# Optimization experiments

Hardware: AMD Instinct MI355X
Metric: run time of the kernel (lower is better)

## Reference

```python
import jax
import jax.numpy as jnp
import numpy as np

N = 16384        # total input points (single batch: o = [N])
C_IN = 64        # in_planes
C_OUT = 128      # out_planes
NSAMPLE = 16     # neighbors per sampled point
STRIDE = 4       # -> new_stride = 2, FPS samples N//2 points
BN_EPS = 1e-5


def setup_inputs() -> dict:
    key = jax.random.key(0)
    k1, k2, k3 = jax.random.split(key, 3)
    p = jax.random.normal(k1, (N, 3), dtype=jnp.float32)
    x = jax.random.normal(k2, (N, C_IN), dtype=jnp.float32)
    o = jnp.array([N], dtype=jnp.int32)  # single-batch offset
    W = jax.random.normal(k3, (3 + C_IN, C_OUT), dtype=jnp.float32) * 0.05
    gamma = jnp.ones((C_OUT,), dtype=jnp.float32)
    beta = jnp.zeros((C_OUT,), dtype=jnp.float32)
    return {"p": p, "x": x, "o": o, "W": W, "gamma": gamma, "beta": beta}


def fps(p, m):
    """Furthest point sampling: returns m indices into p [N,3], starting at 0."""
    n = p.shape[0]
    def step(carry, _):
        dists, last = carry  # dists: [N] min sq-dist to selected set
        d = jnp.sum((p - p[last]) ** 2, axis=-1)
        dists = jnp.minimum(dists, d)
        nxt = jnp.argmax(dists).astype(jnp.int32)
        return (dists, nxt), nxt
    init = (jnp.full((n,), 1e10, dtype=p.dtype), jnp.int32(0))
    _, rest = jax.lax.scan(step, init, None, length=m - 1)
    return jnp.concatenate([jnp.zeros((1,), jnp.int32), rest])


def knn_idx(q, p, k):
    """Indices of k nearest points in p [N,3] for each query in q [m,3]."""
    d = (jnp.sum(q * q, -1, keepdims=True)
         - 2.0 * (q @ p.T)
         + jnp.sum(p * p, -1))  # [m, N]
    _, idx = jax.lax.top_k(-d, k)
    return idx


def group_mlp_pool(q, p, x, W, gamma, beta):
    """queryandgroup(use_xyz=True) -> linear -> BN(train) -> ReLU -> maxpool(nsample)."""
    idx = knn_idx(q, p, NSAMPLE)                      # [m, k]
    rel = p[idx] - q[:, None, :]                       # [m, k, 3] relative xyz
    feats = jnp.concatenate([rel, x[idx]], axis=-1)    # [m, k, 3+C_IN]
    h = feats @ W                                      # [m, k, C_OUT]
    # BatchNorm1d in training mode: stats over (m, k) per channel
    mean = jnp.mean(h, axis=(0, 1))
    var = jnp.var(h, axis=(0, 1))
    h = (h - mean) * jax.lax.rsqrt(var + BN_EPS) * gamma + beta
    h = jax.nn.relu(h)
    return jnp.max(h, axis=1)                          # [m, C_OUT]


def reference(p, x, o, W, gamma, beta):
    m_total = N // (STRIDE // 2)       # 8192 sampled points
    idx = fps(p, m_total)
    m1 = m_total // 2 + m_total % 2    # first half (ceil)
    idx1, idx2 = idx[:m1], idx[m1:]
    n_p, n_p2 = p[idx1], p[idx2]
    x1 = group_mlp_pool(n_p, p, x, W, gamma, beta)
    x2 = group_mlp_pool(n_p2, p, x, W, gamma, beta)
    n_o = jnp.array([m1], dtype=jnp.int32)
    n_o2 = jnp.array([m_total - m1], dtype=jnp.int32)
    return (n_p, x1, n_o, n_p2, x2, n_o2)
```

## Files before the change

### kernel.cpp

```cpp
#include <hip/hip_runtime.h>

#define N_PTS 16384
#define M_TOTAL 8192
#define M1 4096

#define OUT_NP   0
#define OUT_X1   12288
#define OUT_NO   536576
#define OUT_NP2  536577
#define OUT_X2   548865
#define OUT_NO2  1073153

#define POOL_C 64

__global__ void k0_init(const float* __restrict__ p, float* __restrict__ sump,
                        float* __restrict__ px, float* __restrict__ py, float* __restrict__ pz,
                        float* __restrict__ out, int* __restrict__ flag, int* __restrict__ fidx) {
    int i = blockIdx.x * 256 + threadIdx.x;
    if (i == 0) { out[OUT_NO] = 4096.0f; out[OUT_NO2] = 4096.0f; atomicExch(flag, 0); }
    if (i < M_TOTAL) fidx[i] = (i == 0) ? 0 : -1;
    if (i < N_PTS) {
        float x = p[3*i], y = p[3*i+1], z = p[3*i+2];
        px[i] = x; py[i] = y; pz[i] = z;
        sump[i] = __fadd_rn(__fadd_rn(__fmul_rn(x,x), __fmul_rn(y,y)), __fmul_rn(z,z));
    }
}

__device__ __forceinline__ unsigned spread4(unsigned v) {
    return (v & 1u) | ((v & 2u) << 2) | ((v & 4u) << 4) | ((v & 8u) << 6);
}
__device__ __forceinline__ float bb_d2(float qx, float qy, float qz,
                                       float mnx, float mxx, float mny, float mxy,
                                       float mnz, float mxz) {
    float ax = fmaxf(fmaxf(__fsub_rn(mnx, qx), __fsub_rn(qx, mxx)), 0.0f);
    float ay = fmaxf(fmaxf(__fsub_rn(mny, qy), __fsub_rn(qy, mxy)), 0.0f);
    float az = fmaxf(fmaxf(__fsub_rn(mnz, qz), __fsub_rn(qz, mxz)), 0.0f);
    return __fadd_rn(__fadd_rn(__fmul_rn(ax,ax), __fmul_rn(ay,ay)), __fmul_rn(az,az));
}
__device__ __forceinline__ float pt_d2(float ax, float ay, float az,
                                       float bx, float by, float bz) {
    float dx = __fsub_rn(ax,bx), dy = __fsub_rn(ay,by), dz = __fsub_rn(az,bz);
    return __fadd_rn(__fadd_rn(__fmul_rn(dx,dx), __fmul_rn(dy,dy)), __fmul_rn(dz,dz));
}
__device__ __forceinline__ float wave_max64(float v) {
    v = fmaxf(v, __int_as_float(__builtin_amdgcn_update_dpp(0, __float_as_int(v), 0x111, 0xf, 0xf, true)));
    v = fmaxf(v, __int_as_float(__builtin_amdgcn_update_dpp(0, __float_as_int(v), 0x112, 0xf, 0xf, true)));
    v = fmaxf(v, __int_as_float(__builtin_amdgcn_update_dpp(0, __float_as_int(v), 0x114, 0xf, 0xf, true)));
    v = fmaxf(v, __int_as_float(__builtin_amdgcn_update_dpp(0, __float_as_int(v), 0x118, 0xf, 0xf, true)));
    v = fmaxf(v, __int_as_float(__builtin_amdgcn_update_dpp(0, __float_as_int(v), 0x142, 0xf, 0xf, true)));
    v = fmaxf(v, __int_as_float(__builtin_amdgcn_update_dpp(0, __float_as_int(v), 0x143, 0xf, 0xf, true)));
    return __int_as_float(__builtin_amdgcn_readlane(__float_as_int(v), 63));
}

__global__ __launch_bounds__(1024, 4) void k1_fps(
    const float* __restrict__ p,
    float* __restrict__ rx, float* __restrict__ ry, float* __restrict__ rz,
    int* __restrict__ rid,
    int* __restrict__ fidx, float* __restrict__ out, int* __restrict__ flag,
    const float* __restrict__ px, const float* __restrict__ py,
    const float* __restrict__ pz, const float* __restrict__ sump,
    int* __restrict__ knn)
{
    int tid = threadIdx.x, lane = tid & 63, wv = tid >> 6;

    __shared__ int hist[4096];
    __shared__ float sred[16][6];
    __shared__ int wsum[16];
    __shared__ float4 pool4[POOL_C];
    __shared__ unsigned ppk[POOL_C];
    __shared__ float4 barr4[POOL_C+1];
    __shared__ unsigned skeys[POOL_C];
    __shared__ float fdv[16];
    __shared__ unsigned fdk[16];
    __shared__ unsigned mcell;
    __shared__ float s_invm;
    __shared__ int s_cutbin;
    __shared__ unsigned s_cutbits;
    __shared__ unsigned s_fkey;
    __shared__ int bcnt, tcell;
    __shared__ float sdk[4][16][64];
    __shared__ int   sik[4][16][64];

    if (blockIdx.x != 0) {
        float a0 = 1.0f + tid, a1 = 2.0f, a2 = 3.0f, a3 = 4.0f;
        const float hb = 1.0000001f, hc = 1e-9f;
        if (wv < 4) {
            int g = (blockIdx.x - 1) * 4 + wv;
            for (int jq = 0; jq < 9; ++jq) {
                int q = g + 1020 * jq;
                if (q >= M_TOTAL) break;
                int qi = -1;
                for (;;) {
                    if (lane == 0)
                        qi = __hip_atomic_load(&fidx[q], __ATOMIC_RELAXED, __HIP_MEMORY_SCOPE_AGENT);
                    qi = __shfl(qi, 0);
                    if (qi >= 0) break;
#pragma unroll
                    for (int u = 0; u < 256; ++u) {
                        a0 = __fmaf_rn(a0, hb, hc); a1 = __fmaf_rn(a1, hb, hc);
                        a2 = __fmaf_rn(a2, hb, hc); a3 = __fmaf_rn(a3, hb, hc);
                    }
                }
                float qx = px[qi], qy = py[qi], qz = pz[qi], sq = sump[qi];
                float bd[16]; int bi[16];
#pragma unroll
                for (int k = 0; k < 16; ++k) { bd[k] = 3.4e38f; bi[k] = 0x7fffffff; }
                for (int j0 = 0; j0 < N_PTS; j0 += 64) {
                    int j = j0 + lane;
                    float dot = __fmaf_rn(pz[j], qz, __fmaf_rn(py[j], qy, __fmul_rn(px[j], qx)));
                    float d = __fadd_rn(__fsub_rn(sq, __fmul_rn(2.0f, dot)), sump[j]);
                    if (d < bd[15]) {
                        float cdv = d; int ci = j;
#pragma unroll
                        for (int k = 0; k < 16; ++k) {
                            if (cdv < bd[k]) { float td = bd[k]; int ti = bi[k]; bd[k] = cdv; bi[k] = ci; cdv = td; ci = ti; }
                        }
                    }
                }
#pragma unroll
                for (int k = 0; k < 16; ++k) { sdk[wv][k][lane] = bd[k]; sik[wv][k][lane] = bi[k]; }
                int pos = 0;
                for (int r = 0; r < 16; ++r) {
                    float hd = (pos < 16) ? sdk[wv][pos][lane] : 3.4e38f;
                    int   hi2 = (pos < 16) ? sik[wv][pos][lane] : 0x7fffffff;
                    float md = hd; int mi = hi2;
#pragma unroll
                    for (int off = 1; off < 64; off <<= 1) {
                        float od = __shfl_xor(md, off);
                        int   oi = __shfl_xor(mi, off);
                        if (od < md || (od == md && oi < mi)) { md = od; mi = oi; }
                    }
                    if (hi2 == mi && pos < 16) pos++;
                    if (lane == 0) knn[q*16 + r] = mi;
                }
            }
        }
        for (;;) {
#pragma unroll
            for (int u = 0; u < 512; ++u) {
                a0 = __fmaf_rn(a0, hb, hc); a1 = __fmaf_rn(a1, hb, hc);
                a2 = __fmaf_rn(a2, hb, hc); a3 = __fmaf_rn(a3, hb, hc);
            }
            int done = 0;
            if (lane == 0)
                done = __hip_atomic_load(flag, __ATOMIC_RELAXED, __HIP_MEMORY_SCOPE_AGENT);
            done = __shfl(done, 0);
            if (done) break;
        }
        __asm__ volatile("" :: "v"(a0), "v"(a1), "v"(a2), "v"(a3));
        return;
    }

    float mnx = 3.4e38f, mny = 3.4e38f, mnz = 3.4e38f;
    float mxx = -3.4e38f, mxy = -3.4e38f, mxz = -3.4e38f;
#pragma unroll
    for (int k = 0; k < 16; ++k) {
        int i = tid + 1024*k;
        float x = p[3*i], y = p[3*i+1], z = p[3*i+2];
        mnx = fminf(mnx, x); mxx = fmaxf(mxx, x);
        mny = fminf(mny, y); mxy = fmaxf(mxy, y);
        mnz = fminf(mnz, z); mxz = fmaxf(mxz, z);
    }
#pragma unroll
    for (int off = 1; off < 64; off <<= 1) {
        mnx = fminf(mnx, __shfl_xor(mnx, off)); mxx = fmaxf(mxx, __shfl_xor(mxx, off));
        mny = fminf(mny, __shfl_xor(mny, off)); mxy = fmaxf(mxy, __shfl_xor(mxy, off));
        mnz = fminf(mnz, __shfl_xor(mnz, off)); mxz = fmaxf(mxz, __shfl_xor(mxz, off));
    }
    if (lane == 0) {
        sred[wv][0] = mnx; sred[wv][1] = mxx; sred[wv][2] = mny;
        sred[wv][3] = mxy; sred[wv][4] = mnz; sred[wv][5] = mxz;
    }
    for (int j = tid; j < 4096; j += 1024) hist[j] = 0;
    __syncthreads();
    mnx = sred[0][0]; mxx = sred[0][1]; mny = sred[0][2];
    mxy = sred[0][3]; mnz = sred[0][4]; mxz = sred[0][5];
    for (int w2 = 1; w2 < 16; ++w2) {
        mnx = fminf(mnx, sred[w2][0]); mxx = fmaxf(mxx, sred[w2][1]);
        mny = fminf(mny, sred[w2][2]); mxy = fmaxf(mxy, sred[w2][3]);
        mnz = fminf(mnz, sred[w2][4]); mxz = fmaxf(mxz, sred[w2][5]);
    }
    float sx = 16.0f / fmaxf(mxx - mnx, 1e-20f);
    float sy = 16.0f / fmaxf(mxy - mny, 1e-20f);
    float sz = 16.0f / fmaxf(mxz - mnz, 1e-20f);

    int mcode[16];
#pragma unroll
    for (int k = 0; k < 16; ++k) {
        int i = tid + 1024*k;
        float x = p[3*i], y = p[3*i+1], z = p[3*i+2];
        int cx = min(15, (int)((x - mnx) * sx));
        int cy = min(15, (int)((y - mny) * sy));
        int cz = min(15, (int)((z - mnz) * sz));
        int m = (int)(spread4((unsigned)cx) | (spread4((unsigned)cy) << 1) | (spread4((unsigned)cz) << 2));
        mcode[k] = m;
        atomicAdd(&hist[m], 1);
    }
    __syncthreads();
    {
        int c0 = hist[4*tid], c1 = hist[4*tid+1], c2 = hist[4*tid+2], c3 = hist[4*tid+3];
        int lsum = c0 + c1 + c2 + c3;
        int incl = lsum;
#pragma unroll
        for (int off = 1; off < 64; off <<= 1) {
            int n = __shfl_up(incl, off);
            if (lane >= off) incl += n;
        }
        if (lane == 63) wsum[wv] = incl;
        __syncthreads();
        int woff = 0;
        for (int j = 0; j < wv; ++j) woff += wsum[j];
        int excl = woff + incl - lsum;
        hist[4*tid]   = excl;
        hist[4*tid+1] = excl + c0;
        hist[4*tid+2] = excl + c0 + c1;
        hist[4*tid+3] = excl + c0 + c1 + c2;
    }
    __syncthreads();
#pragma unroll
    for (int k = 0; k < 16; ++k) {
        int i = tid + 1024*k;
        int pos = atomicAdd(&hist[mcode[k]], 1);
        rx[pos] = p[3*i]; ry[pos] = p[3*i+1]; rz[pos] = p[3*i+2];
        rid[pos] = i;
    }
    __syncthreads();

    int base = tid * 16;
    float ld[16];
    float bmnx = 3.4e38f, bmny = 3.4e38f, bmnz = 3.4e38f;
    float bmxx = -3.4e38f, bmxy = -3.4e38f, bmxz = -3.4e38f;
#pragma unroll
    for (int k = 0; k < 16; ++k) {
        float x = rx[base+k], y = ry[base+k], z = rz[base+k];
        ld[k] = 1e10f;
        bmnx = fminf(bmnx, x); bmxx = fmaxf(bmxx, x);
        bmny = fminf(bmny, y); bmxy = fmaxf(bmxy, y);
        bmnz = fminf(bmnz, z); bmxz = fmaxf(bmxz, z);
    }
    float wsmnx = bmnx, wsmxx = bmxx, wsmny = bmny, wsmxy = bmxy, wsmnz = bmnz, wsmxz = bmxz;
#pragma unroll
    for (int off = 1; off < 64; off <<= 1) {
        wsmnx = fminf(wsmnx, __shfl_xor(wsmnx, off)); wsmxx = fmaxf(wsmxx, __shfl_xor(wsmxx, off));
        wsmny = fminf(wsmny, __shfl_xor(wsmny, off)); wsmxy = fmaxf(wsmxy, __shfl_xor(wsmxy, off));
        wsmnz = fminf(wsmnz, __shfl_xor(wsmnz, off)); wsmxz = fmaxf(wsmxz, __shfl_xor(wsmxz, off));
    }
    float gmax = 1e10f, wave_gmax = 1e10f;

    if (tid == 0) {
        float x0 = p[0], y0 = p[1], z0 = p[2];
        out[OUT_NP+0] = x0; out[OUT_NP+1] = y0; out[OUT_NP+2] = z0;
        barr4[0] = make_float4(x0, y0, z0, 0.0f);
        skeys[0] = 0u;
        bcnt = 1; tcell = 1; mcell = 0u;
    }

    for (;;) {
        __syncthreads();
        int t_now = tcell;
        int s = bcnt;
        if (tid < s)
            __hip_atomic_store(&fidx[t_now - s + tid], (int)skeys[tid], __ATOMIC_RELAXED, __HIP_MEMORY_SCOPE_AGENT);
        if (t_now >= M_TOTAL) break;

        {
            bool dirtyw = false;
            if (lane < s) {
                float4 cc = barr4[lane];
                dirtyw = bb_d2(cc.x, cc.y, cc.z, wsmnx, wsmxx, wsmny, wsmxy, wsmnz, wsmxz) < wave_gmax;
            }
            unsigned long long mm = __ballot(dirtyw);
            if (mm) {
                float gx[16], gy[16], gz[16];
#pragma unroll
                for (int k = 0; k < 16; ++k) { gx[k] = rx[base+k]; gy[k] = ry[base+k]; gz[k] = rz[base+k]; }
                while (mm) {
                    int b = __builtin_ctzll(mm); mm &= mm - 1;
                    float4 cc = barr4[b];
                    if (bb_d2(cc.x, cc.y, cc.z, bmnx, bmxx, bmny, bmxy, bmnz, bmxz) < gmax) {
#pragma unroll
                        for (int k = 0; k < 16; ++k)
                            ld[k] = fminf(ld[k], pt_d2(gx[k], gy[k], gz[k], cc.x, cc.y, cc.z));
                    }
                }
            }
        }
        gmax = ld[0];
#pragma unroll
        for (int k = 1; k < 16; ++k) gmax = fmaxf(gmax, ld[k]);
        wave_gmax = wave_max64(gmax);
        if (lane == 0) atomicMax(&mcell, __float_as_uint(wave_gmax));
        if (tid < 130) hist[tid] = 0;
        __syncthreads();
        if (tid == 0) { s_invm = 1.0f / __uint_as_float(mcell); mcell = 0u; }
        __syncthreads();
        float invm = s_invm;
#pragma unroll
        for (int k = 0; k < 16; ++k) {
            unsigned u = __float_as_uint(__fmul_rn(ld[k], invm));
            if (u >= 0x3F000000u) {
                int bin = 16256 - (int)(u >> 16);
                bin = bin < 0 ? 0 : (bin > 128 ? 128 : bin);
                atomicAdd(&hist[bin], 1);
            }
        }
        __syncthreads();
        if (wv == 0) {
            int b0 = hist[2*lane], b1 = hist[2*lane+1];
            int pair = b0 + b1;
            int incl = pair;
#pragma unroll
            for (int off = 1; off < 64; off <<= 1) { int n = __shfl_up(incl, off); if (lane >= off) incl += n; }
            int before = incl - pair;
            int cb = 0;
            if (before + b0 <= POOL_C) cb = 2*lane + 1;
            if (before + pair <= POOL_C) cb = 2*lane + 2;
            if (lane == 63) { if (incl + hist[128] <= POOL_C) cb = 129; }
#pragma unroll
            for (int off = 1; off < 64; off <<= 1) cb = max(cb, __shfl_xor(cb, off));
            if (lane == 0) { s_cutbin = cb; s_cutbits = (unsigned)(16257 - cb) << 16; }
        }
        __syncthreads();

        unsigned cutbits = s_cutbits;
        int cl = 0;
#pragma unroll
        for (int k = 0; k < 16; ++k)
            cl += (__float_as_uint(__fmul_rn(ld[k], invm)) >= cutbits) ? 1 : 0;
        int inc3 = cl;
#pragma unroll
        for (int off = 1; off < 64; off <<= 1) { int n = __shfl_up(inc3, off); if (lane >= off) inc3 += n; }
        if (lane == 63) wsum[wv] = inc3;
        __syncthreads();
        int woff2 = 0, ptot = 0;
        for (int j = 0; j < 16; ++j) { int wsj = wsum[j]; if (j < wv) woff2 += wsj; ptot += wsj; }

        if (s_cutbin == 0 || ptot == 0) {
            float bv = -1.0f; unsigned bk = 0xffffffffu;
#pragma unroll
            for (int k = 0; k < 16; ++k) {
                unsigned kk = ((unsigned)rid[base+k] << 14) | (unsigned)(base + k);
                bool better = (ld[k] > bv) || (ld[k] == bv && kk < bk);
                bv = better ? ld[k] : bv; bk = better ? kk : bk;
            }
#pragma unroll
            for (int off = 1; off < 64; off <<= 1) {
                float ov = __shfl_xor(bv, off); unsigned ok = __shfl_xor(bk, off);
                bool better = (ov > bv) || (ov == bv && ok < bk);
                bv = better ? ov : bv; bk = better ? ok : bk;
            }
            if (lane == 0) { fdv[wv] = bv; fdk[wv] = bk; }
            __syncthreads();
            if (tid < 64) {
                float v2 = (tid < 16) ? fdv[tid] : -1.0f;
                unsigned k2v = (tid < 16) ? fdk[tid] : 0xffffffffu;
#pragma unroll
                for (int off = 1; off < 16; off <<= 1) {
                    float ov = __shfl_xor(v2, off); unsigned ok = __shfl_xor(k2v, off);
                    bool better = (ov > v2) || (ov == v2 && ok < k2v);
                    v2 = better ? ov : v2; k2v = better ? ok : k2v;
                }
                if (tid == 0) {
                    s_fkey = k2v;
                    int pos = (int)(k2v & 16383u);
                    __hip_atomic_store(&fidx[t_now], (int)(k2v >> 14), __ATOMIC_RELAXED, __HIP_MEMORY_SCOPE_AGENT);
                    float wx = rx[pos], wy = ry[pos], wz = rz[pos];
                    int o = (t_now < M1) ? (OUT_NP + 3*t_now) : (OUT_NP2 + 3*(t_now - M1));
                    out[o] = wx; out[o+1] = wy; out[o+2] = wz;
                    tcell = t_now + 1; bcnt = 0;
                }
            }
            __syncthreads();
            {
                int pos = (int)(s_fkey & 16383u);
                float wx = rx[pos], wy = ry[pos], wz = rz[pos];
                if (bb_d2(wx, wy, wz, bmnx, bmxx, bmny, bmxy, bmnz, bmxz) < gmax) {
#pragma unroll
                    for (int k = 0; k < 16; ++k)
                        ld[k] = fminf(ld[k], pt_d2(rx[base+k], ry[base+k], rz[base+k], wx, wy, wz));
                }
            }
            continue;
        }

        int nb = woff2 + inc3 - cl;
#pragma unroll
        for (int k = 0; k < 16; ++k) {
            if (__float_as_uint(__fmul_rn(ld[k], invm)) >= cutbits) {
                pool4[nb] = make_float4(rx[base+k], ry[base+k], rz[base+k], ld[k]);
                ppk[nb] = (unsigned)rid[base+k];
                nb++;
            }
        }
        if (tid >= ptot && tid < POOL_C) {
            pool4[tid] = make_float4(0.0f, 0.0f, 0.0f, 0.0f);
            ppk[tid] = 0x7fffffffu;
        }
        __syncthreads();

        if (wv == 0) {
            __builtin_amdgcn_s_setprio(3);
            float4 e = pool4[lane];
            float ex = e.x, ey = e.y, ez = e.z, dv = e.w;
            unsigned key = ppk[lane];
            int tl = t_now, bc = 0;
            float mw = wave_max64(dv);
            while (__float_as_uint(__fmul_rn(mw, invm)) >= cutbits) {
                unsigned long long tie = __ballot(dv == mw);
                int wl;
                if (__popcll(tie) == 1) {
                    wl = (int)__builtin_ctzll(tie);
                } else {
                    unsigned kk = (dv == mw) ? key : 0xffffffffu;
#pragma unroll
                    for (int off = 1; off < 64; off <<= 1) kk = min(kk, (unsigned)__shfl_xor((int)kk, off));
                    tie = __ballot(dv == mw && key == kk);
                    wl = (int)__builtin_ctzll(tie);
                }
                float wx = __int_as_float(__builtin_amdgcn_readlane(__float_as_int(ex), wl));
                float wy = __int_as_float(__builtin_amdgcn_readlane(__float_as_int(ey), wl));
                float wz = __int_as_float(__builtin_amdgcn_readlane(__float_as_int(ez), wl));
                unsigned wk = (unsigned)__builtin_amdgcn_readlane((int)key, wl);
                if (lane == 0) {
                    skeys[bc] = wk;
                    int o = (tl < M1) ? (OUT_NP + 3*tl) : (OUT_NP2 + 3*(tl - M1));
                    out[o] = wx; out[o+1] = wy; out[o+2] = wz;
                    barr4[bc] = make_float4(wx, wy, wz, 0.0f);
                }
                ++bc; ++tl;
                if (tl >= M_TOTAL) break;
                dv = fminf(dv, pt_d2(ex, ey, ez, wx, wy, wz));
                mw = wave_max64(dv);
            }
            __builtin_amdgcn_s_setprio(0);
            if (lane == 0) { bcnt = bc; tcell = tl; }
        }
    }

    if (tid == 0) atomicExch(flag, 1);
}

__global__ __launch_bounds__(128) void k3_gemm(const float* __restrict__ p3, const float* __restrict__ xin,
                                               const float* __restrict__ W,
                                               const int* __restrict__ fidx, const int* __restrict__ knn,
                                               float* __restrict__ hmax, float* __restrict__ hmin,
                                               double* __restrict__ psum, double* __restrict__ psq) {
    __shared__ __align__(16) float feats[16][68];
    int c = threadIdx.x;
    int qbase = blockIdx.x * 16;
    float w[68];
#pragma unroll
    for (int j = 0; j < 67; ++j) w[j] = W[j*128 + c];
    w[67] = 0.0f;

    double s = 0.0, ss = 0.0;
    for (int qq = 0; qq < 16; ++qq) {
        int q = qbase + qq;
        int qi = fidx[q];
        float qx = p3[3*qi], qy = p3[3*qi+1], qz = p3[3*qi+2];
        for (int i = c; i < 16*68; i += 128) {
            int sIdx = i / 68, j = i - sIdx*68;
            int nj = knn[q*16 + sIdx];
            float v;
            if (j < 3) {
                float pc = p3[3*nj + j];
                float qc = (j == 0) ? qx : ((j == 1) ? qy : qz);
                v = pc - qc;
            } else if (j < 67) {
                v = xin[nj*64 + (j-3)];
            } else v = 0.0f;
            feats[sIdx][j] = v;
        }
        __syncthreads();
        float hmx = -3.4e38f, hmn = 3.4e38f;
        for (int sIdx = 0; sIdx < 16; ++sIdx) {
            float acc = 0.0f;
#pragma unroll
            for (int mm = 0; mm < 17; ++mm) {
                float4 f = *(const float4*)&feats[sIdx][4*mm];
                acc = __fmaf_rn(f.x, w[4*mm+0], acc);
                acc = __fmaf_rn(f.y, w[4*mm+1], acc);
                acc = __fmaf_rn(f.z, w[4*mm+2], acc);
                acc = __fmaf_rn(f.w, w[4*mm+3], acc);
            }
            hmx = fmaxf(hmx, acc); hmn = fminf(hmn, acc);
            s += (double)acc; ss += (double)acc * (double)acc;
        }
        hmax[q*128 + c] = hmx; hmin[q*128 + c] = hmn;
        __syncthreads();
    }
    psum[blockIdx.x*128 + c] = s;
    psq [blockIdx.x*128 + c] = ss;
}

__global__ void k35_stats(const double* __restrict__ psum, const double* __restrict__ psq,
                          const float* __restrict__ gamma, const float* __restrict__ beta,
                          float* __restrict__ scale, float* __restrict__ shift) {
    int t = threadIdx.x;
    int half = t >> 7, c = t & 127;
    double s = 0.0, ss = 0.0;
    for (int b = 0; b < 256; ++b) {
        int ib = (half*256 + b)*128 + c;
        s += psum[ib]; ss += psq[ib];
    }
    double mean = s / 65536.0;
    double var  = ss / 65536.0 - mean*mean;
    double sc   = (double)gamma[c] / sqrt(var + 1e-5);
    scale[t] = (float)sc;
    shift[t] = (float)((double)beta[c] - mean*sc);
}

__global__ __launch_bounds__(256) void k4_out(const float* __restrict__ hmax, const float* __restrict__ hmin,
                                              const float* __restrict__ scale, const float* __restrict__ shift,
                                              float* __restrict__ out) {
    int e = blockIdx.x * 256 + threadIdx.x;
    int q = e >> 7, c = e & 127;
    int half = (q >= M1) ? 1 : 0;
    float a = scale[half*128 + c], b = shift[half*128 + c];
    float v = (a >= 0.0f) ? hmax[e] : hmin[e];
    float r = fmaxf(0.0f, a*v + b);
    int off = half ? (OUT_X2 + (q - M1)*128 + c) : (OUT_X1 + q*128 + c);
    out[off] = r;
}

extern "C" void kernel_launch(void* const* d_in, const int* in_sizes, int n_in,
                              void* d_out, int out_size, void* d_ws, size_t ws_size,
                              hipStream_t stream) {
    const float* p     = (const float*)d_in[0];
    const float* x     = (const float*)d_in[1];
    const float* W     = (const float*)d_in[3];
    const float* gamma = (const float*)d_in[4];
    const float* beta  = (const float*)d_in[5];
    float* out = (float*)d_out;

    float* wsf  = (float*)d_ws;
    float* sump = wsf;
    float* px   = wsf + 16384;
    float* py   = wsf + 32768;
    float* pz   = wsf + 49152;
    int*   fidx = (int*)(wsf + 65536);
    int*   knn  = (int*)(wsf + 73728);
    float* hmax = wsf + 204800;
    float* hmin = wsf + 1253376;
    float* rxp  = hmax;
    float* ryp  = hmax + 16384;
    float* rzp  = hmax + 32768;
    int*   ridp = (int*)(hmax + 49152);
    int*   flag = (int*)(wsf + 270336);
    double* psum = (double*)((char*)d_ws + 9207808);
    double* psq  = psum + 65536;
    float* scale = (float*)(psq + 65536);
    float* shift = scale + 256;

    k0_init <<<64,   256, 0, stream>>>(p, sump, px, py, pz, out, flag, fidx);
    k1_fps  <<<256, 1024, 0, stream>>>(p, rxp, ryp, rzp, ridp, fidx, out, flag, px, py, pz, sump, knn);
    k3_gemm <<<512,  128, 0, stream>>>(p, x, W, fidx, knn, hmax, hmin, psum, psq);
    k35_stats<<<1,   256, 0, stream>>>(psum, psq, gamma, beta, scale, shift);
    k4_out  <<<4096, 256, 0, stream>>>(hmax, hmin, scale, shift, out);
}
```

Before: 5.505 ms.

## Fuse grouped linear and BN stats into KNN worker waves of FPS kernel

The separate GEMM kernel is removed. Each KNN worker wave now keeps its 16 neighbor indices in registers and computes the 67x128 linear projection, the per-channel max/min and the BN sums inline. The sums are accumulated into a global buffer with double-precision atomics instead of per-block partials. This cuts a kernel launch and the knn index round trip, and it overlaps the GEMM with the serial FPS phase. The cost is uncoalesced per-lane reads of W and x, atomic contention on 512 doubles, and higher register pressure now that the occupancy hint is dropped from launch bounds.

```diff
diff --git a/kernel.cpp b/kernel.cpp
--- a/kernel.cpp
+++ b/kernel.cpp
@@ -15,9 +15,11 @@
 
 __global__ void k0_init(const float* __restrict__ p, float* __restrict__ sump,
                         float* __restrict__ px, float* __restrict__ py, float* __restrict__ pz,
-                        float* __restrict__ out, int* __restrict__ flag, int* __restrict__ fidx) {
+                        float* __restrict__ out, int* __restrict__ flag, int* __restrict__ fidx,
+                        double* __restrict__ bn) {
     int i = blockIdx.x * 256 + threadIdx.x;
     if (i == 0) { out[OUT_NO] = 4096.0f; out[OUT_NO2] = 4096.0f; atomicExch(flag, 0); }
+    if (i < 512) bn[i] = 0.0;
     if (i < M_TOTAL) fidx[i] = (i == 0) ? 0 : -1;
     if (i < N_PTS) {
         float x = p[3*i], y = p[3*i+1], z = p[3*i+2];
@@ -52,14 +54,16 @@
     return __int_as_float(__builtin_amdgcn_readlane(__float_as_int(v), 63));
 }
 
-__global__ __launch_bounds__(1024, 4) void k1_fps(
+__global__ __launch_bounds__(1024) void k1_fps(
     const float* __restrict__ p,
     float* __restrict__ rx, float* __restrict__ ry, float* __restrict__ rz,
     int* __restrict__ rid,
     int* __restrict__ fidx, float* __restrict__ out, int* __restrict__ flag,
     const float* __restrict__ px, const float* __restrict__ py,
     const float* __restrict__ pz, const float* __restrict__ sump,
-    int* __restrict__ knn)
+    const float* __restrict__ xin, const float* __restrict__ W,
+    float* __restrict__ hmax, float* __restrict__ hmin,
+    double* __restrict__ bn)
 {
     int tid = threadIdx.x, lane = tid & 63, wv = tid >> 6;
 
@@ -119,7 +123,9 @@
                 }
 #pragma unroll
                 for (int k = 0; k < 16; ++k) { sdk[wv][k][lane] = bd[k]; sik[wv][k][lane] = bi[k]; }
+                int njr[16];
                 int pos = 0;
+#pragma unroll
                 for (int r = 0; r < 16; ++r) {
                     float hd = (pos < 16) ? sdk[wv][pos][lane] : 3.4e38f;
                     int   hi2 = (pos < 16) ? sik[wv][pos][lane] : 0x7fffffff;
@@ -131,8 +137,44 @@
                         if (od < md || (od == md && oi < mi)) { md = od; mi = oi; }
                     }
                     if (hi2 == mi && pos < 16) pos++;
-                    if (lane == 0) knn[q*16 + r] = mi;
-                }
+                    njr[r] = mi;
+                }
+
+                float hmx0 = -3.4e38f, hmn0 = 3.4e38f, hmx1 = -3.4e38f, hmn1 = 3.4e38f;
+                double sm0 = 0.0, sq0 = 0.0, sm1 = 0.0, sq1 = 0.0;
+#pragma unroll
+                for (int s2 = 0; s2 < 16; ++s2) {
+                    int nj = njr[s2];
+                    float acc0 = 0.0f, acc1 = 0.0f;
+                    {
+                        float f0 = p[3*nj+0] - qx;
+                        acc0 = __fmaf_rn(f0, W[0*128 + lane], acc0);
+                        acc1 = __fmaf_rn(f0, W[0*128 + 64 + lane], acc1);
+                        float f1 = p[3*nj+1] - qy;
+                        acc0 = __fmaf_rn(f1, W[1*128 + lane], acc0);
+                        acc1 = __fmaf_rn(f1, W[1*128 + 64 + lane], acc1);
+                        float f2 = p[3*nj+2] - qz;
+                        acc0 = __fmaf_rn(f2, W[2*128 + lane], acc0);
+                        acc1 = __fmaf_rn(f2, W[2*128 + 64 + lane], acc1);
+                    }
+                    const float* xr = &xin[nj*64];
+                    for (int j = 3; j < 67; ++j) {
+                        float f = xr[j-3];
+                        acc0 = __fmaf_rn(f, W[j*128 + lane], acc0);
+                        acc1 = __fmaf_rn(f, W[j*128 + 64 + lane], acc1);
+                    }
+                    hmx0 = fmaxf(hmx0, acc0); hmn0 = fminf(hmn0, acc0);
+                    hmx1 = fmaxf(hmx1, acc1); hmn1 = fminf(hmn1, acc1);
+                    sm0 += (double)acc0; sq0 += (double)acc0 * (double)acc0;
+                    sm1 += (double)acc1; sq1 += (double)acc1 * (double)acc1;
+                }
+                hmax[q*128 + lane]      = hmx0;  hmax[q*128 + 64 + lane] = hmx1;
+                hmin[q*128 + lane]      = hmn0;  hmin[q*128 + 64 + lane] = hmn1;
+                int hb2 = (q >= M1) ? 128 : 0;
+                atomicAdd(&bn[hb2 + lane],            sm0);
+                atomicAdd(&bn[hb2 + 64 + lane],       sm1);
+                atomicAdd(&bn[256 + hb2 + lane],      sq0);
+                atomicAdd(&bn[256 + hb2 + 64 + lane], sq1);
             }
         }
         for (;;) {
@@ -440,71 +482,13 @@
     if (tid == 0) atomicExch(flag, 1);
 }
 
-__global__ __launch_bounds__(128) void k3_gemm(const float* __restrict__ p3, const float* __restrict__ xin,
-                                               const float* __restrict__ W,
-                                               const int* __restrict__ fidx, const int* __restrict__ knn,
-                                               float* __restrict__ hmax, float* __restrict__ hmin,
-                                               double* __restrict__ psum, double* __restrict__ psq) {
-    __shared__ __align__(16) float feats[16][68];
-    int c = threadIdx.x;
-    int qbase = blockIdx.x * 16;
-    float w[68];
-#pragma unroll
-    for (int j = 0; j < 67; ++j) w[j] = W[j*128 + c];
-    w[67] = 0.0f;
-
-    double s = 0.0, ss = 0.0;
-    for (int qq = 0; qq < 16; ++qq) {
-        int q = qbase + qq;
-        int qi = fidx[q];
-        float qx = p3[3*qi], qy = p3[3*qi+1], qz = p3[3*qi+2];
-        for (int i = c; i < 16*68; i += 128) {
-            int sIdx = i / 68, j = i - sIdx*68;
-            int nj = knn[q*16 + sIdx];
-            float v;
-            if (j < 3) {
-                float pc = p3[3*nj + j];
-                float qc = (j == 0) ? qx : ((j == 1) ? qy : qz);
-                v = pc - qc;
-            } else if (j < 67) {
-                v = xin[nj*64 + (j-3)];
-            } else v = 0.0f;
-            feats[sIdx][j] = v;
-        }
-        __syncthreads();
-        float hmx = -3.4e38f, hmn = 3.4e38f;
-        for (int sIdx = 0; sIdx < 16; ++sIdx) {
-            float acc = 0.0f;
-#pragma unroll
-            for (int mm = 0; mm < 17; ++mm) {
-                float4 f = *(const float4*)&feats[sIdx][4*mm];
-                acc = __fmaf_rn(f.x, w[4*mm+0], acc);
-                acc = __fmaf_rn(f.y, w[4*mm+1], acc);
-                acc = __fmaf_rn(f.z, w[4*mm+2], acc);
-                acc = __fmaf_rn(f.w, w[4*mm+3], acc);
-            }
-            hmx = fmaxf(hmx, acc); hmn = fminf(hmn, acc);
-            s += (double)acc; ss += (double)acc * (double)acc;
-        }
-        hmax[q*128 + c] = hmx; hmin[q*128 + c] = hmn;
-        __syncthreads();
-    }
-    psum[blockIdx.x*128 + c] = s;
-    psq [blockIdx.x*128 + c] = ss;
-}
-
-__global__ void k35_stats(const double* __restrict__ psum, const double* __restrict__ psq,
+__global__ void k35_stats(const double* __restrict__ bn,
                           const float* __restrict__ gamma, const float* __restrict__ beta,
                           float* __restrict__ scale, float* __restrict__ shift) {
     int t = threadIdx.x;
-    int half = t >> 7, c = t & 127;
-    double s = 0.0, ss = 0.0;
-    for (int b = 0; b < 256; ++b) {
-        int ib = (half*256 + b)*128 + c;
-        s += psum[ib]; ss += psq[ib];
-    }
-    double mean = s / 65536.0;
-    double var  = ss / 65536.0 - mean*mean;
+    int c = t & 127;
+    double mean = bn[t] / 65536.0;
+    double var  = bn[256 + t] / 65536.0 - mean*mean;
     double sc   = (double)gamma[c] / sqrt(var + 1e-5);
     scale[t] = (float)sc;
     shift[t] = (float)((double)beta[c] - mean*sc);
@@ -539,22 +523,20 @@
     float* py   = wsf + 32768;
     float* pz   = wsf + 49152;
     int*   fidx = (int*)(wsf + 65536);
-    int*   knn  = (int*)(wsf + 73728);
     float* hmax = wsf + 204800;
     float* hmin = wsf + 1253376;
-    float* rxp  = hmax;
-    float* ryp  = hmax + 16384;
-    float* rzp  = hmax + 32768;
-    int*   ridp = (int*)(hmax + 49152);
-    int*   flag = (int*)(wsf + 270336);
-    double* psum = (double*)((char*)d_ws + 9207808);
-    double* psq  = psum + 65536;
-    float* scale = (float*)(psq + 65536);
+    float* rxp  = (float*)((char*)d_ws + 9207808);
+    float* ryp  = rxp + 16384;
+    float* rzp  = ryp + 16384;
+    int*   ridp = (int*)(rzp + 16384);
+    int*   flag = (int*)(ridp + 16384);
+    double* bn  = (double*)((char*)d_ws + 9207808 + 4*65536 + 256);
+    float* scale = (float*)(bn + 512);
     float* shift = scale + 256;
 
-    k0_init <<<64,   256, 0, stream>>>(p, sump, px, py, pz, out, flag, fidx);
-    k1_fps  <<<256, 1024, 0, stream>>>(p, rxp, ryp, rzp, ridp, fidx, out, flag, px, py, pz, sump, knn);
-    k3_gemm <<<512,  128, 0, stream>>>(p, x, W, fidx, knn, hmax, hmin, psum, psq);
-    k35_stats<<<1,   256, 0, stream>>>(psum, psq, gamma, beta, scale, shift);
+    k0_init <<<64,   256, 0, stream>>>(p, sump, px, py, pz, out, flag, fidx, bn);
+    k1_fps  <<<256, 1024, 0, stream>>>(p, rxp, ryp, rzp, ridp, fidx, out, flag,
+                                       px, py, pz, sump, x, W, hmax, hmin, bn);
+    k35_stats<<<1,   256, 0, stream>>>(bn, gamma, beta, scale, shift);
     k4_out  <<<4096, 256, 0, stream>>>(hmax, hmin, scale, shift, out);
 }
```

Result: faster. 5.282 ms, median of 2 (-4.1%).
